# Optimization experiments

Measured on AMD Instinct MI355X. Metric: run time of the kernel, lower is better.

The kernel has to match this reference:

```python
import jax, jax.numpy as jnp
import numpy as np

COS_MARGIN = 0.35
ARC_MARGIN = 0.5
SCALE = 30.0
EPS = 1e-12

B, V = 2048, 32000


def setup_inputs() -> dict:
    key = jax.random.key(0)
    k1, k2 = jax.random.split(key)
    # logits are cosine similarities in [-1, 1]
    preds = jax.random.uniform(k1, (B, V), dtype=jnp.float32) * 2.0 - 1.0
    labels = jax.random.randint(k2, (B,), 0, V, dtype=jnp.int64)
    return {"preds": preds, "labels": labels}


def reference(preds, labels):
    # target cosine: preds[i, labels[i]]  (torch.diagonal(preds.T[labels]))
    target = jnp.take_along_axis(preds, labels[:, None], axis=1)[:, 0]
    theta = jnp.arccos(jnp.clip(target, -1.0 + EPS, 1.0 - EPS))
    theta = jnp.clip(theta, EPS, jnp.pi - EPS)  # 4*arctan(1) == pi
    numerator = SCALE * (jnp.cos(theta + ARC_MARGIN) - COS_MARGIN)  # [B]
    # sum of exp(scale * preds) over all classes except the target class
    cols = jnp.arange(preds.shape[1])  # [V]
    exp_all = jnp.exp(SCALE * preds)  # [B, V]
    sum_others = jnp.sum(jnp.where(cols[None, :] == labels[:, None], 0.0, exp_all), axis=1)
    denominator = jnp.exp(numerator) + sum_others
    return -jnp.mean(numerator - jnp.log(denominator))
```

## Files before the change

### kernel.cpp

```cpp
#include <hip/hip_runtime.h>
#include <math.h>

#define B_ROWS 2048
#define V_COLS 32000
#define SCALE_D 30.0
#define COS_MARGIN_D 0.35
#define ARC_MARGIN_D 0.5
#define EPS_D 1e-12
#define PI_D 3.14159265358979323846

#define LOG2E_X30 43.2808512266689022212f

typedef float f32x4 __attribute__((ext_vector_type(4)));

#define TPB 1024

__global__ __launch_bounds__(TPB) void cosarc_row_kernel(
    const float* __restrict__ preds,
    const int*   __restrict__ labels,
    float*       __restrict__ row_terms)
{
    const int row = blockIdx.x;
    const int tid = threadIdx.x;
    const float* rowp = preds + (size_t)row * V_COLS;
    const f32x4* p4 = (const f32x4*)rowp;

    f32x4 v0 = __builtin_nontemporal_load(&p4[tid]);
    f32x4 v1 = __builtin_nontemporal_load(&p4[tid + 1 * TPB]);
    f32x4 v2 = __builtin_nontemporal_load(&p4[tid + 2 * TPB]);
    f32x4 v3 = __builtin_nontemporal_load(&p4[tid + 3 * TPB]);
    f32x4 v4 = __builtin_nontemporal_load(&p4[tid + 4 * TPB]);
    f32x4 v5 = __builtin_nontemporal_load(&p4[tid + 5 * TPB]);
    f32x4 v6 = __builtin_nontemporal_load(&p4[tid + 6 * TPB]);
    const bool has8 = (tid < (V_COLS / 4 - 7 * TPB));
    f32x4 v7 = {0.f, 0.f, 0.f, 0.f};
    if (has8) v7 = __builtin_nontemporal_load(&p4[tid + 7 * TPB]);

    #define EXP30(x) __builtin_amdgcn_exp2f((x) * LOG2E_X30)

    float sx, sy, sz, sw;
    sx  = EXP30(v0.x); sy  = EXP30(v0.y); sz  = EXP30(v0.z); sw  = EXP30(v0.w);
    sx += EXP30(v1.x); sy += EXP30(v1.y); sz += EXP30(v1.z); sw += EXP30(v1.w);
    sx += EXP30(v2.x); sy += EXP30(v2.y); sz += EXP30(v2.z); sw += EXP30(v2.w);
    sx += EXP30(v3.x); sy += EXP30(v3.y); sz += EXP30(v3.z); sw += EXP30(v3.w);
    sx += EXP30(v4.x); sy += EXP30(v4.y); sz += EXP30(v4.z); sw += EXP30(v4.w);
    sx += EXP30(v5.x); sy += EXP30(v5.y); sz += EXP30(v5.z); sw += EXP30(v5.w);
    sx += EXP30(v6.x); sy += EXP30(v6.y); sz += EXP30(v6.z); sw += EXP30(v6.w);
    if (has8) {
        sx += EXP30(v7.x); sy += EXP30(v7.y); sz += EXP30(v7.z); sw += EXP30(v7.w);
    }

    double sum = (double)((sx + sy) + (sz + sw));

    #pragma unroll
    for (int off = 32; off > 0; off >>= 1)
        sum += __shfl_down(sum, off, 64);

    __shared__ double wave_sums[TPB / 64];
    const int wave = tid >> 6;
    const int lane = tid & 63;
    if (lane == 0) wave_sums[wave] = sum;
    __syncthreads();

    if (tid == 0) {
        double total = 0.0;
        #pragma unroll
        for (int w = 0; w < TPB / 64; ++w) total += wave_sums[w];

        const float tgt_f = rowp[labels[row]];
        const double sum_others =
            total - (double)EXP30(tgt_f);

        double t = (double)tgt_f;
        t = fmin(fmax(t, -1.0 + EPS_D), 1.0 - EPS_D);
        double theta = acos(t);
        theta = fmin(fmax(theta, EPS_D), PI_D - EPS_D);
        const double numerator = SCALE_D * (cos(theta + ARC_MARGIN_D) - COS_MARGIN_D);
        const double denominator = exp(numerator) + sum_others;
        row_terms[row] = (float)(numerator - log(denominator));
    }
}

__global__ __launch_bounds__(256) void cosarc_reduce_kernel(
    const float* __restrict__ row_terms,
    float*       __restrict__ out)
{
    const int tid = threadIdx.x;
    double s = 0.0;
    for (int i = tid; i < B_ROWS; i += 256)
        s += (double)row_terms[i];

    #pragma unroll
    for (int off = 32; off > 0; off >>= 1)
        s += __shfl_down(s, off, 64);

    __shared__ double wave_sums[4];
    if ((tid & 63) == 0) wave_sums[tid >> 6] = s;
    __syncthreads();

    if (tid == 0) {
        double total = wave_sums[0] + wave_sums[1] + wave_sums[2] + wave_sums[3];
        out[0] = (float)(-(total / (double)B_ROWS));
    }
}

extern "C" void kernel_launch(void* const* d_in, const int* in_sizes, int n_in,
                              void* d_out, int out_size, void* d_ws, size_t ws_size,
                              hipStream_t stream)
{
    const float* preds  = (const float*)d_in[0];
    const int*   labels = (const int*)d_in[1];
    float*       out    = (float*)d_out;
    float*       ws     = (float*)d_ws;

    cosarc_row_kernel<<<B_ROWS, TPB, 0, stream>>>(preds, labels, ws);
    cosarc_reduce_kernel<<<1, 256, 0, stream>>>(ws, out);
}
```

Before: 325.0 us.

## Shrink row blocks to 256 threads and stream each row through rotating register buffers

Each row block drops from 1024 to 256 threads, and each thread now walks 31 strided float4 chunks plus a tail. It keeps four loads in flight and issues the next load right after consuming a buffer, instead of loading all eight chunks up front. The aim is to keep more small blocks resident per CU and to hide memory latency with a steady software pipeline. The cost is that each thread does more serial work, and fewer threads cover each row.

```diff
diff --git a/kernel.cpp b/kernel.cpp
--- a/kernel.cpp
+++ b/kernel.cpp
@@ -13,7 +13,10 @@
 
 typedef float f32x4 __attribute__((ext_vector_type(4)));
 
-#define TPB 1024
+#define TPB 256
+
+#define NT(p) __builtin_nontemporal_load(&(p))
+#define EXP30(x) __builtin_amdgcn_exp2f((x) * LOG2E_X30)
 
 __global__ __launch_bounds__(TPB) void cosarc_row_kernel(
     const float* __restrict__ preds,
@@ -25,30 +28,34 @@
     const float* rowp = preds + (size_t)row * V_COLS;
     const f32x4* p4 = (const f32x4*)rowp;
 
-    f32x4 v0 = __builtin_nontemporal_load(&p4[tid]);
-    f32x4 v1 = __builtin_nontemporal_load(&p4[tid + 1 * TPB]);
-    f32x4 v2 = __builtin_nontemporal_load(&p4[tid + 2 * TPB]);
-    f32x4 v3 = __builtin_nontemporal_load(&p4[tid + 3 * TPB]);
-    f32x4 v4 = __builtin_nontemporal_load(&p4[tid + 4 * TPB]);
-    f32x4 v5 = __builtin_nontemporal_load(&p4[tid + 5 * TPB]);
-    f32x4 v6 = __builtin_nontemporal_load(&p4[tid + 6 * TPB]);
-    const bool has8 = (tid < (V_COLS / 4 - 7 * TPB));
-    f32x4 v7 = {0.f, 0.f, 0.f, 0.f};
-    if (has8) v7 = __builtin_nontemporal_load(&p4[tid + 7 * TPB]);
+    f32x4 b0 = NT(p4[0 * TPB + tid]);
+    f32x4 b1 = NT(p4[1 * TPB + tid]);
+    f32x4 b2 = NT(p4[2 * TPB + tid]);
+    f32x4 b3 = NT(p4[3 * TPB + tid]);
+    const bool hastail = (tid < (V_COLS / 4 - 31 * TPB));
+    f32x4 bt = {0.f, 0.f, 0.f, 0.f};
+    if (hastail) bt = NT(p4[31 * TPB + tid]);
 
-    #define EXP30(x) __builtin_amdgcn_exp2f((x) * LOG2E_X30)
+    float sx = 0.f, sy = 0.f, sz = 0.f, sw = 0.f;
+#define CONSUME(v)                                                   \
+    do {                                                             \
+        sx += EXP30((v).x); sy += EXP30((v).y);                      \
+        sz += EXP30((v).z); sw += EXP30((v).w);                      \
+    } while (0)
 
-    float sx, sy, sz, sw;
-    sx  = EXP30(v0.x); sy  = EXP30(v0.y); sz  = EXP30(v0.z); sw  = EXP30(v0.w);
-    sx += EXP30(v1.x); sy += EXP30(v1.y); sz += EXP30(v1.z); sw += EXP30(v1.w);
-    sx += EXP30(v2.x); sy += EXP30(v2.y); sz += EXP30(v2.z); sw += EXP30(v2.w);
-    sx += EXP30(v3.x); sy += EXP30(v3.y); sz += EXP30(v3.z); sw += EXP30(v3.w);
-    sx += EXP30(v4.x); sy += EXP30(v4.y); sz += EXP30(v4.z); sw += EXP30(v4.w);
-    sx += EXP30(v5.x); sy += EXP30(v5.y); sz += EXP30(v5.z); sw += EXP30(v5.w);
-    sx += EXP30(v6.x); sy += EXP30(v6.y); sz += EXP30(v6.z); sw += EXP30(v6.w);
-    if (has8) {
-        sx += EXP30(v7.x); sy += EXP30(v7.y); sz += EXP30(v7.z); sw += EXP30(v7.w);
+    for (int k = 0; k + 8 <= 31; k += 4) {
+        CONSUME(b0); b0 = NT(p4[(k + 4) * TPB + tid]);
+        CONSUME(b1); b1 = NT(p4[(k + 5) * TPB + tid]);
+        CONSUME(b2); b2 = NT(p4[(k + 6) * TPB + tid]);
+        CONSUME(b3); b3 = NT(p4[(k + 7) * TPB + tid]);
     }
+    CONSUME(b0); b0 = NT(p4[28 * TPB + tid]);
+    CONSUME(b1); b1 = NT(p4[29 * TPB + tid]);
+    CONSUME(b2); b2 = NT(p4[30 * TPB + tid]);
+    CONSUME(b3);
+    CONSUME(b0); CONSUME(b1); CONSUME(b2);
+    if (hastail) CONSUME(bt);
+#undef CONSUME
 
     double sum = (double)((sx + sy) + (sz + sw));
 
@@ -68,8 +75,7 @@
         for (int w = 0; w < TPB / 64; ++w) total += wave_sums[w];
 
         const float tgt_f = rowp[labels[row]];
-        const double sum_others =
-            total - (double)EXP30(tgt_f);
+        const double sum_others = total - (double)EXP30(tgt_f);
 
         double t = (double)tgt_f;
         t = fmin(fmax(t, -1.0 + EPS_D), 1.0 - EPS_D);
```

Result: no change. 323.5 us (-0.5%).
